# Kernel optimization log

Hardware: AMD Instinct MI355X
Metric: run time of the kernel (lower is better)

Reference implementation:

```python
import jax, jax.numpy as jnp
import numpy as np

QDIM = 1024; KDIM = 2048; NH = 16; HD = QDIM // NH
H = 64; W = 64; B = 8; S2 = 256
EPS = 1e-6; SCALE = HD ** -0.5


def setup_inputs() -> dict:
    key = jax.random.key(0)
    ks = jax.random.split(key, 8)
    def lin(k, fan_in, shape):
        lim = 1.0 / np.sqrt(fan_in)
        return jax.random.uniform(k, shape, jnp.float32, -lim, lim)
    return {
        "x": jax.random.normal(ks[0], (B, H * W, QDIM), jnp.float32),
        "y": jax.random.normal(ks[1], (B, S2, KDIM), jnp.float32),
        "wq": lin(ks[2], QDIM, (QDIM, QDIM)),
        "bq": lin(ks[3], QDIM, (QDIM,)),
        "wkv": lin(ks[4], KDIM, (2 * QDIM, KDIM)),
        "bkv": lin(ks[5], KDIM, (2 * QDIM,)),
        "wo": lin(ks[6], QDIM, (QDIM, QDIM)),
        "bo": lin(ks[7], QDIM, (QDIM,)),
        "qn_g": jnp.ones((HD,), jnp.float32),
        "qn_b": jnp.zeros((HD,), jnp.float32),
        "kn_g": jnp.ones((HD,), jnp.float32),
        "kn_b": jnp.zeros((HD,), jnp.float32),
    }


def _layernorm(t, g, b):
    mu = t.mean(-1, keepdims=True)
    var = ((t - mu) ** 2).mean(-1, keepdims=True)
    return (t - mu) * jax.lax.rsqrt(var + EPS) * g + b


def _rope_2d_angles():
    # Lumina-style 2D rotary: head_dim//2 complex freqs per position,
    # interleaving H-axis and W-axis frequencies along the pair dim.
    d4 = HD // 4
    inv = 1.0 / (10000.0 ** (np.arange(0, HD // 2, 2, dtype=np.float32) / (HD // 2)))  # (d4,)
    fh = np.outer(np.arange(H, dtype=np.float32), inv)  # (H, d4)
    fw = np.outer(np.arange(W, dtype=np.float32), inv)  # (W, d4)
    ang = np.stack([
        np.broadcast_to(fh[:, None, :], (H, W, d4)),
        np.broadcast_to(fw[None, :, :], (H, W, d4)),
    ], axis=-1).reshape(H, W, HD // 2)  # interleaved h,w,h,w,...
    return jnp.asarray(np.cos(ang)), jnp.asarray(np.sin(ang))


def reference(x, y, wq, bq, wkv, bkv, wo, bo, qn_g, qn_b, kn_g, kn_b):
    b, s1, c = x.shape
    q = (x @ wq.T + bq).reshape(b, s1, NH, HD).transpose(0, 2, 1, 3)          # (b, nh, s1, hd)
    kv = (y @ wkv.T + bkv).reshape(b, -1, 2, NH, HD).transpose(0, 2, 3, 1, 4)  # (b, 2, nh, s2, hd)
    k, v = kv[:, 0], kv[:, 1]
    q = _layernorm(q, qn_g, qn_b)
    k = _layernorm(k, kn_g, kn_b)
    # inline 2D RoPE on Q only (complex mult on interleaved pairs)
    cos, sin = _rope_2d_angles()                                               # (H, W, hd//2)
    qr = q.reshape(b, NH, H, W, HD // 2, 2)
    qe, qo = qr[..., 0], qr[..., 1]
    q = jnp.stack([qe * cos - qo * sin, qe * sin + qo * cos], axis=-1).reshape(b, NH, s1, HD)
    attn = jax.nn.softmax((q * SCALE) @ jnp.swapaxes(k, -2, -1), axis=-1)      # (b, nh, s1, s2)
    out = (attn @ v).transpose(0, 2, 1, 3).reshape(b, s1, c)
    return out @ wo.T + bo
```

## Files before the change

### kernel.cpp

```cpp
#include <hip/hip_runtime.h>
#include <hip/hip_bf16.h>

typedef __bf16 bf16x8 __attribute__((ext_vector_type(8)));
typedef __bf16 bf16x4 __attribute__((ext_vector_type(4)));
typedef float f32x4 __attribute__((ext_vector_type(4)));

__device__ __forceinline__ void async_copy16(__bf16* lds_base, const __bf16* g) {
  __builtin_amdgcn_global_load_lds(
      (const __attribute__((address_space(1))) void*)g,
      (__attribute__((address_space(3))) void*)lds_base, 16, 0, 0);
}

__global__ __launch_bounds__(256) void cvt_bf16(const float* __restrict__ in,
                                                __bf16* __restrict__ out, int n4) {
  int i = blockIdx.x * 256 + threadIdx.x;
  if (i >= n4) return;
  float4 v = ((const float4*)in)[i];
  bf16x4 o;
  o.x = (__bf16)v.x; o.y = (__bf16)v.y; o.z = (__bf16)v.z; o.w = (__bf16)v.w;
  ((bf16x4*)out)[i] = o;
}

template<bool STORE_BF16>
__global__ __launch_bounds__(256) void gemm_bt(const __bf16* __restrict__ A,
                                               const __bf16* __restrict__ Bw,
                                               const float* __restrict__ bias,
                                               void* __restrict__ Cp,
                                               int M, int N, int K) {
  __shared__ __align__(16) __bf16 sA[128 * 64];
  __shared__ __align__(16) __bf16 sB[128 * 64];
  const int tid = threadIdx.x;
  const int lane = tid & 63;
  const int w = tid >> 6;
  const int wr = w >> 1, wc = w & 1;
  const int l15 = lane & 15, q4 = lane >> 4;
  const int bm = blockIdx.x, bn = blockIdx.y;

  f32x4 acc[4][4] = {};

  for (int k0 = 0; k0 < K; k0 += 64) {
    __syncthreads();
#pragma unroll
    for (int it = 0; it < 4; ++it) {
      int chunk = it * 256 + tid;
      int row = chunk >> 3, c8 = chunk & 7;
      int ldsbase = (it * 256 + w * 64) * 8;
      async_copy16(sA + ldsbase, A + (size_t)(bm * 128 + row) * K + k0 + c8 * 8);
      async_copy16(sB + ldsbase, Bw + (size_t)(bn * 128 + row) * K + k0 + c8 * 8);
    }
    __syncthreads();
#pragma unroll
    for (int kk = 0; kk < 2; ++kk) {
      bf16x8 af[4], bfr[4];
#pragma unroll
      for (int i = 0; i < 4; ++i)
        af[i] = *(const bf16x8*)(sA + (wr * 64 + i * 16 + l15) * 64 + kk * 32 + q4 * 8);
#pragma unroll
      for (int j = 0; j < 4; ++j)
        bfr[j] = *(const bf16x8*)(sB + (wc * 64 + j * 16 + l15) * 64 + kk * 32 + q4 * 8);
#pragma unroll
      for (int i = 0; i < 4; ++i)
#pragma unroll
        for (int j = 0; j < 4; ++j)
          acc[i][j] = __builtin_amdgcn_mfma_f32_16x16x32_bf16(af[i], bfr[j], acc[i][j], 0, 0, 0);
    }
  }
#pragma unroll
  for (int j = 0; j < 4; ++j) {
    const int col = bn * 128 + wc * 64 + j * 16 + l15;
    const float bv = bias[col];
#pragma unroll
    for (int i = 0; i < 4; ++i) {
      const int row0 = bm * 128 + wr * 64 + i * 16 + q4 * 4;
#pragma unroll
      for (int r = 0; r < 4; ++r) {
        float v = acc[i][j][r] + bv;
        size_t off = (size_t)(row0 + r) * N + col;
        if (STORE_BF16) ((__bf16*)Cp)[off] = (__bf16)v;
        else            ((float*)Cp)[off]  = v;
      }
    }
  }
}

template<int KK, int EPI>
__global__ __launch_bounds__(512, 2) void gemm_big(const __bf16* __restrict__ A,
                                                   const __bf16* __restrict__ Bw,
                                                   const float* __restrict__ bias,
                                                   void* __restrict__ Cp,
                                                   const float* __restrict__ g,
                                                   const float* __restrict__ bt,
                                                   int N) {
  constexpr int NT = KK / 64;
  static_assert(NT >= 3, "need >=3 K-tiles");
  __shared__ __align__(16) __bf16 sA[2][256 * 64];
  __shared__ __align__(16) __bf16 sB[2][256 * 64];
  const int tid = threadIdx.x;
  const int lane = tid & 63;
  const int w = tid >> 6;
  const int wr = w >> 2, wc = w & 3;
  const int l15 = lane & 15, q4 = lane >> 4;
  const int bm = blockIdx.x, bn = blockIdx.y;

  const int rl = lane >> 3;
  const int cs = (lane & 7) ^ rl;
  const __bf16* Ag = A + (size_t)(bm * 256) * KK + cs * 8;
  const __bf16* Bg = Bw + (size_t)(bn * 256) * KK + cs * 8;
  const int gbA = w * 8;
  const int gbB = (w & 3) * 8 + (w >> 2) * 64;

  auto STAGE_A = [&](int bb, int t, int h) {
    int gb = gbA + h * 64;
    async_copy16(&sA[bb][gb * 64],         Ag + (size_t)(gb + rl) * KK + t * 64);
    async_copy16(&sA[bb][(gb + 128) * 64], Ag + (size_t)(gb + 128 + rl) * KK + t * 64);
  };
  auto STAGE_B = [&](int bb, int t, int h) {
    int gb = gbB + h * 32;
    async_copy16(&sB[bb][gb * 64],         Bg + (size_t)(gb + rl) * KK + t * 64);
    async_copy16(&sB[bb][(gb + 128) * 64], Bg + (size_t)(gb + 128 + rl) * KK + t * 64);
  };

  const int pc0 = ((q4) ^ (l15 & 7)) * 8;
  const int pc1 = ((4 + q4) ^ (l15 & 7)) * 8;
  const int arow0 = (wr * 128 + l15) * 64;
  const int brow0 = (wc * 64 + l15) * 64;

  f32x4 acc[8][4] = {};

  STAGE_A(0, 0, 0); STAGE_B(0, 0, 0); STAGE_B(0, 0, 1); STAGE_A(0, 0, 1);
  STAGE_A(1, 1, 0); STAGE_B(1, 1, 0);
  asm volatile("s_waitcnt vmcnt(4)" ::: "memory");
  __builtin_amdgcn_s_barrier();
  __builtin_amdgcn_sched_barrier(0);

#pragma unroll 2
  for (int t = 0; t < NT; ++t) {
    const int cb = t & 1, nb = cb ^ 1;
    const __bf16* sAc = sA[cb];
    const __bf16* sBc = sB[cb];
    bf16x8 a[4][2], b0[2][2], b1[2][2];

#pragma unroll
    for (int m = 0; m < 4; ++m) {
      a[m][0] = *(const bf16x8*)(sAc + arow0 + m * 1024 + pc0);
      a[m][1] = *(const bf16x8*)(sAc + arow0 + m * 1024 + pc1);
    }
#pragma unroll
    for (int n = 0; n < 2; ++n) {
      b0[n][0] = *(const bf16x8*)(sBc + brow0 + n * 1024 + pc0);
      b0[n][1] = *(const bf16x8*)(sBc + brow0 + n * 1024 + pc1);
    }
    if (t + 1 < NT) STAGE_B(nb, t + 1, 1);
    __builtin_amdgcn_s_barrier();
    asm volatile("s_waitcnt lgkmcnt(0)" ::: "memory");
    __builtin_amdgcn_sched_barrier(0);
    __builtin_amdgcn_s_setprio(1);
#pragma unroll
    for (int m = 0; m < 4; ++m)
#pragma unroll
      for (int n = 0; n < 2; ++n) {
        acc[m][n] = __builtin_amdgcn_mfma_f32_16x16x32_bf16(a[m][0], b0[n][0], acc[m][n], 0, 0, 0);
        acc[m][n] = __builtin_amdgcn_mfma_f32_16x16x32_bf16(a[m][1], b0[n][1], acc[m][n], 0, 0, 0);
      }
    __builtin_amdgcn_s_setprio(0);
    __builtin_amdgcn_s_barrier();
    __builtin_amdgcn_sched_barrier(0);

#pragma unroll
    for (int n = 0; n < 2; ++n) {
      b1[n][0] = *(const bf16x8*)(sBc + brow0 + (2 + n) * 1024 + pc0);
      b1[n][1] = *(const bf16x8*)(sBc + brow0 + (2 + n) * 1024 + pc1);
    }
    if (t + 1 < NT) STAGE_A(nb, t + 1, 1);
    __builtin_amdgcn_s_barrier();
    asm volatile("s_waitcnt lgkmcnt(0)" ::: "memory");
    __builtin_amdgcn_sched_barrier(0);
    __builtin_amdgcn_s_setprio(1);
#pragma unroll
    for (int m = 0; m < 4; ++m)
#pragma unroll
      for (int n = 0; n < 2; ++n) {
        acc[m][2 + n] = __builtin_amdgcn_mfma_f32_16x16x32_bf16(a[m][0], b1[n][0], acc[m][2 + n], 0, 0, 0);
        acc[m][2 + n] = __builtin_amdgcn_mfma_f32_16x16x32_bf16(a[m][1], b1[n][1], acc[m][2 + n], 0, 0, 0);
      }
    __builtin_amdgcn_s_setprio(0);
    __builtin_amdgcn_s_barrier();
    __builtin_amdgcn_sched_barrier(0);

#pragma unroll
    for (int m = 0; m < 4; ++m) {
      a[m][0] = *(const bf16x8*)(sAc + arow0 + (4 + m) * 1024 + pc0);
      a[m][1] = *(const bf16x8*)(sAc + arow0 + (4 + m) * 1024 + pc1);
    }
    if (t + 2 < NT) STAGE_A(cb, t + 2, 0);
    __builtin_amdgcn_s_barrier();
    asm volatile("s_waitcnt lgkmcnt(0)" ::: "memory");
    __builtin_amdgcn_sched_barrier(0);
    __builtin_amdgcn_s_setprio(1);
#pragma unroll
    for (int m = 0; m < 4; ++m)
#pragma unroll
      for (int n = 0; n < 2; ++n) {
        acc[4 + m][n] = __builtin_amdgcn_mfma_f32_16x16x32_bf16(a[m][0], b0[n][0], acc[4 + m][n], 0, 0, 0);
        acc[4 + m][n] = __builtin_amdgcn_mfma_f32_16x16x32_bf16(a[m][1], b0[n][1], acc[4 + m][n], 0, 0, 0);
      }
    __builtin_amdgcn_s_setprio(0);
    __builtin_amdgcn_s_barrier();
    __builtin_amdgcn_sched_barrier(0);

    if (t + 2 < NT) STAGE_B(cb, t + 2, 0);
    if (t + 2 < NT)      { asm volatile("s_waitcnt vmcnt(4)" ::: "memory"); }
    else if (t + 1 < NT) { asm volatile("s_waitcnt vmcnt(0)" ::: "memory"); }
    __builtin_amdgcn_s_barrier();
    __builtin_amdgcn_sched_barrier(0);
    __builtin_amdgcn_s_setprio(1);
#pragma unroll
    for (int m = 0; m < 4; ++m)
#pragma unroll
      for (int n = 0; n < 2; ++n) {
        acc[4 + m][2 + n] = __builtin_amdgcn_mfma_f32_16x16x32_bf16(a[m][0], b1[n][0], acc[4 + m][2 + n], 0, 0, 0);
        acc[4 + m][2 + n] = __builtin_amdgcn_mfma_f32_16x16x32_bf16(a[m][1], b1[n][1], acc[4 + m][2 + n], 0, 0, 0);
      }
    __builtin_amdgcn_s_setprio(0);
    __builtin_amdgcn_s_barrier();
    __builtin_amdgcn_sched_barrier(0);
  }

  if (EPI == 0) {
#pragma unroll
    for (int n = 0; n < 4; ++n) {
      const int col = bn * 256 + wc * 64 + n * 16 + l15;
      const float bv = bias[col];
#pragma unroll
      for (int m = 0; m < 8; ++m) {
        const int row0 = bm * 256 + wr * 128 + m * 16 + q4 * 4;
#pragma unroll
        for (int r = 0; r < 4; ++r)
          ((float*)Cp)[(size_t)(row0 + r) * N + col] = acc[m][n][r] + bv;
      }
    }
  } else {
    const int nh = bn * 4 + wc;
    const int usew = (l15 >> 1) & 1;
    const float sgn = (l15 & 1) ? 1.f : -1.f;
    float gq[4], bqv[4], inv[4], bv[4];
#pragma unroll
    for (int n = 0; n < 4; ++n) {
      const int d = n * 16 + l15;
      gq[n] = g[d]; bqv[n] = bt[d];
      bv[n] = bias[nh * 64 + d];
      inv[n] = __expf(-(float)(d >> 2) * 0.5756462732485114f);
    }
#pragma unroll
    for (int m = 0; m < 8; ++m) {
#pragma unroll
      for (int r = 0; r < 4; ++r) {
        const int row = bm * 256 + wr * 128 + m * 16 + q4 * 4 + r;
        const int s1 = row & 4095, bidx = row >> 12;
        const float base = usew ? (float)(s1 & 63) : (float)(s1 >> 6);
        float v[4];
        float sum = 0.f;
#pragma unroll
        for (int n = 0; n < 4; ++n) { v[n] = acc[m][n][r] + bv[n]; sum += v[n]; }
        sum += __shfl_xor(sum, 1); sum += __shfl_xor(sum, 2);
        sum += __shfl_xor(sum, 4); sum += __shfl_xor(sum, 8);
        const float mu = sum * (1.f / 64.f);
        float sq = 0.f;
#pragma unroll
        for (int n = 0; n < 4; ++n) { v[n] -= mu; sq += v[n] * v[n]; }
        sq += __shfl_xor(sq, 1); sq += __shfl_xor(sq, 2);
        sq += __shfl_xor(sq, 4); sq += __shfl_xor(sq, 8);
        const float rs = rsqrtf(sq * (1.f / 64.f) + 1e-6f);
        __bf16* Qrow = (__bf16*)Cp + ((size_t)(bidx * 16 + nh) * 4096 + s1) * 64;
#pragma unroll
        for (int n = 0; n < 4; ++n) {
          const float xn = v[n] * rs * gq[n] + bqv[n];
          const float ang = base * inv[n];
          const float cc = __cosf(ang), ssn = __sinf(ang);
          const float partner = __shfl_xor(xn, 1);
          const float rot = (xn * cc + partner * ssn * sgn) * 0.125f;
          Qrow[n * 16 + l15] = (__bf16)rot;
        }
      }
    }
  }
}

__global__ __launch_bounds__(256) void kv_epilogue(const float* __restrict__ kv,
                                                   const float* __restrict__ g,
                                                   const float* __restrict__ bta,
                                                   __bf16* __restrict__ Kd,
                                                   __bf16* __restrict__ VT) {
  const int lane = threadIdx.x & 63;
  const int vec = blockIdx.x * 4 + (threadIdx.x >> 6);
  const int nh = vec & 15;
  const int sv = (vec >> 4) & 1;
  const int row = vec >> 5;
  const int b = row >> 8, s2 = row & 255;
  float v = kv[(size_t)row * 2048 + sv * 1024 + nh * 64 + lane];
  if (sv == 0) {
    float mu = v;
#pragma unroll
    for (int o = 32; o; o >>= 1) mu += __shfl_xor(mu, o);
    mu *= (1.f / 64.f);
    float d = v - mu;
    float va = d * d;
#pragma unroll
    for (int o = 32; o; o >>= 1) va += __shfl_xor(va, o);
    va *= (1.f / 64.f);
    float xn = d * rsqrtf(va + 1e-6f) * g[lane] + bta[lane];
    Kd[(((size_t)b * 16 + nh) * 256 + s2) * 64 + lane] = (__bf16)xn;
  } else {
    VT[(((size_t)b * 16 + nh) * 64 + lane) * 256 + s2] = (__bf16)v;
  }
}

__global__ __launch_bounds__(256) void attn_kernel(const __bf16* __restrict__ Q,
                                                   const __bf16* __restrict__ Kd,
                                                   const __bf16* __restrict__ VT,
                                                   __bf16* __restrict__ O) {
  __shared__ __align__(16) __bf16 sK[256 * 64];
  __shared__ __align__(16) __bf16 sV[64 * 256];
  const int tid = threadIdx.x, lane = tid & 63, w = tid >> 6;
  const int l15 = lane & 15, q4 = lane >> 4;
  const int s7 = l15 & 7;
  const int bh = blockIdx.y;
  const int m0 = blockIdx.x * 64;
  const __bf16* Kg = Kd + (size_t)bh * 256 * 64;
  const __bf16* Vg = VT + (size_t)bh * 64 * 256;
  const __bf16* Qg = Q + ((size_t)bh * 4096 + m0) * 64;
#pragma unroll
  for (int it = 0; it < 8; ++it) {
    int c = it * 256 + tid;
    int kr = c >> 3, kh = c & 7;
    *(uint4*)(sK + kr * 64 + ((kh ^ (kr & 7)) * 8)) = *(const uint4*)(Kg + c * 8);
    int vr = c >> 5, vh = c & 31;
    *(uint4*)(sV + vr * 256 + ((vh ^ (vr & 7)) * 8)) = *(const uint4*)(Vg + c * 8);
  }
  bf16x8 qf0 = *(const bf16x8*)(Qg + (w * 16 + l15) * 64 + q4 * 8);
  bf16x8 qf1 = *(const bf16x8*)(Qg + (w * 16 + l15) * 64 + 32 + q4 * 8);
  __syncthreads();
  f32x4 sacc[16] = {};
#pragma unroll
  for (int mt = 0; mt < 16; ++mt) {
    bf16x8 a0 = *(const bf16x8*)(sK + (mt * 16 + l15) * 64 + ((q4 ^ s7) * 8));
    bf16x8 a1 = *(const bf16x8*)(sK + (mt * 16 + l15) * 64 + (((4 + q4) ^ s7) * 8));
    sacc[mt] = __builtin_amdgcn_mfma_f32_16x16x32_bf16(a0, qf0, sacc[mt], 0, 0, 0);
    sacc[mt] = __builtin_amdgcn_mfma_f32_16x16x32_bf16(a1, qf1, sacc[mt], 0, 0, 0);
  }
  __syncthreads();
  float mx = -1e30f;
#pragma unroll
  for (int mt = 0; mt < 16; ++mt)
#pragma unroll
    for (int r = 0; r < 4; ++r) mx = fmaxf(mx, sacc[mt][r]);
  mx = fmaxf(mx, __shfl_xor(mx, 16));
  mx = fmaxf(mx, __shfl_xor(mx, 32));
  float l = 0.f;
#pragma unroll
  for (int mt = 0; mt < 16; ++mt)
#pragma unroll
    for (int r = 0; r < 4; ++r) {
      float p = __expf(sacc[mt][r] - mx);
      sacc[mt][r] = p;
      l += p;
    }
  l += __shfl_xor(l, 16);
  l += __shfl_xor(l, 32);
  const float linv = 1.f / l;
#pragma unroll
  for (int mt = 0; mt < 16; ++mt) {
    bf16x4 pk;
    pk.x = (__bf16)(sacc[mt][0] * linv);
    pk.y = (__bf16)(sacc[mt][1] * linv);
    pk.z = (__bf16)(sacc[mt][2] * linv);
    pk.w = (__bf16)(sacc[mt][3] * linv);
    int chunk = mt * 2 + (q4 >> 1);
    *(bf16x4*)(sK + (w * 16 + l15) * 256 + ((chunk ^ s7) * 8) + (q4 & 1) * 4) = pk;
  }
  f32x4 oacc[4] = {};
#pragma unroll
  for (int ks = 0; ks < 8; ++ks) {
    int phys = ((ks * 4 + q4) ^ s7) * 8;
    bf16x8 a = *(const bf16x8*)(sK + (w * 16 + l15) * 256 + phys);
#pragma unroll
    for (int j = 0; j < 4; ++j) {
      bf16x8 b = *(const bf16x8*)(sV + (j * 16 + l15) * 256 + phys);
      oacc[j] = __builtin_amdgcn_mfma_f32_16x16x32_bf16(a, b, oacc[j], 0, 0, 0);
    }
  }
  const int b = bh >> 4, nh = bh & 15;
#pragma unroll
  for (int j = 0; j < 4; ++j)
#pragma unroll
    for (int r = 0; r < 4; ++r) {
      size_t off = ((size_t)b * 4096 + m0 + w * 16 + q4 * 4 + r) * 1024
                 + nh * 64 + j * 16 + l15;
      O[off] = (__bf16)oacc[j][r];
    }
}

extern "C" void kernel_launch(void* const* d_in, const int* in_sizes, int n_in,
                              void* d_out, int out_size, void* d_ws, size_t ws_size,
                              hipStream_t stream) {
  const float* x    = (const float*)d_in[0];
  const float* y    = (const float*)d_in[1];
  const float* wq   = (const float*)d_in[2];
  const float* bq   = (const float*)d_in[3];
  const float* wkv  = (const float*)d_in[4];
  const float* bkv  = (const float*)d_in[5];
  const float* wo   = (const float*)d_in[6];
  const float* bo   = (const float*)d_in[7];
  const float* qng  = (const float*)d_in[8];
  const float* qnb  = (const float*)d_in[9];
  const float* kng  = (const float*)d_in[10];
  const float* knb  = (const float*)d_in[11];
  float* out = (float*)d_out;

  char* ws = (char*)d_ws;
  size_t off = 0;
  auto take = [&](size_t bytes) { char* p = ws + off; off += (bytes + 255) & ~(size_t)255; return p; };
  __bf16* xb   = (__bf16*)take((size_t)32768 * 1024 * 2);
  char*  reg1  = take((size_t)32768 * 1024 * 2);
  __bf16* Qb   = (__bf16*)take((size_t)32768 * 1024 * 2);
  __bf16* yb   = (__bf16*)take((size_t)2048 * 2048 * 2);
  __bf16* wqb  = (__bf16*)take((size_t)1024 * 1024 * 2);
  __bf16* wkvb = (__bf16*)take((size_t)2048 * 2048 * 2);
  __bf16* wob  = (__bf16*)take((size_t)1024 * 1024 * 2);
  __bf16* Kb   = (__bf16*)take((size_t)128 * 256 * 64 * 2);
  __bf16* VTb  = (__bf16*)take((size_t)128 * 64 * 256 * 2);
  float*  kvf  = (float*)reg1;
  __bf16* aout = xb;

  cvt_bf16<<<32768, 256, 0, stream>>>(x,   xb,   8388608);
  cvt_bf16<<<4096,  256, 0, stream>>>(y,   yb,   1048576);
  cvt_bf16<<<1024,  256, 0, stream>>>(wq,  wqb,  262144);
  cvt_bf16<<<4096,  256, 0, stream>>>(wkv, wkvb, 1048576);
  cvt_bf16<<<1024,  256, 0, stream>>>(wo,  wob,  262144);

  gemm_bt<false><<<dim3(16, 16), 256, 0, stream>>>(yb, wkvb, bkv, kvf, 2048, 2048, 2048);
  kv_epilogue<<<16384, 256, 0, stream>>>(kvf, kng, knb, Kb, VTb);

  gemm_big<1024, 2><<<dim3(128, 4), 512, 0, stream>>>(xb, wqb, bq, Qb, qng, qnb, 1024);

  attn_kernel<<<dim3(64, 128), 256, 0, stream>>>(Qb, Kb, VTb, aout);

  gemm_big<1024, 0><<<dim3(128, 4), 512, 0, stream>>>(aout, wob, bo, out, nullptr, nullptr, 1024);
}
```

Measured before the change: 600.0 us.

## Prefetch B fragments, swizzle block order, stage Q epilogue through LDS

Merges the two shared buffers into one array so the Q epilogue can reuse it. Accumulators are written to LDS with an XOR swizzle, and each thread then handles a full 64-wide head row: LayerNorm with no cross-lane shuffles, RoPE, and 16-byte vectorized bf16 stores. The first B fragments of each K-tile are now loaded from LDS at the end of the previous iteration, hiding LDS latency before the MFMAs. The block index is also remapped so consecutive blocks interleave across the grid, aiming for better L2 reuse. The mapping hardcodes grid dimensions (128 columns, 4 bn) and so applies to every gemm_big instantiation, not only the Q projection; it is correct only for those grid sizes.

```diff
diff --git a/kernel.cpp b/kernel.cpp
--- a/kernel.cpp
+++ b/kernel.cpp
@@ -93,14 +93,16 @@
                                                    int N) {
   constexpr int NT = KK / 64;
   static_assert(NT >= 3, "need >=3 K-tiles");
-  __shared__ __align__(16) __bf16 sA[2][256 * 64];
-  __shared__ __align__(16) __bf16 sB[2][256 * 64];
+  __shared__ __align__(16) __bf16 smem[4 * 256 * 64];
   const int tid = threadIdx.x;
   const int lane = tid & 63;
   const int w = tid >> 6;
   const int wr = w >> 2, wc = w & 3;
   const int l15 = lane & 15, q4 = lane >> 4;
-  const int bm = blockIdx.x, bn = blockIdx.y;
+
+  const int bid = (blockIdx.y << 7) + blockIdx.x;
+  const int sbid = (bid & 7) * 64 + (bid >> 3);
+  const int bm = sbid >> 2, bn = sbid & 3;
 
   const int rl = lane >> 3;
   const int cs = (lane & 7) ^ rl;
@@ -109,15 +111,18 @@
   const int gbA = w * 8;
   const int gbB = (w & 3) * 8 + (w >> 2) * 64;
 
+  auto sAbuf = [&](int bb) { return smem + bb * 16384; };
+  auto sBbuf = [&](int bb) { return smem + 32768 + bb * 16384; };
+
   auto STAGE_A = [&](int bb, int t, int h) {
     int gb = gbA + h * 64;
-    async_copy16(&sA[bb][gb * 64],         Ag + (size_t)(gb + rl) * KK + t * 64);
-    async_copy16(&sA[bb][(gb + 128) * 64], Ag + (size_t)(gb + 128 + rl) * KK + t * 64);
+    async_copy16(sAbuf(bb) + gb * 64,         Ag + (size_t)(gb + rl) * KK + t * 64);
+    async_copy16(sAbuf(bb) + (gb + 128) * 64, Ag + (size_t)(gb + 128 + rl) * KK + t * 64);
   };
   auto STAGE_B = [&](int bb, int t, int h) {
     int gb = gbB + h * 32;
-    async_copy16(&sB[bb][gb * 64],         Bg + (size_t)(gb + rl) * KK + t * 64);
-    async_copy16(&sB[bb][(gb + 128) * 64], Bg + (size_t)(gb + 128 + rl) * KK + t * 64);
+    async_copy16(sBbuf(bb) + gb * 64,         Bg + (size_t)(gb + rl) * KK + t * 64);
+    async_copy16(sBbuf(bb) + (gb + 128) * 64, Bg + (size_t)(gb + 128 + rl) * KK + t * 64);
   };
 
   const int pc0 = ((q4) ^ (l15 & 7)) * 8;
@@ -126,30 +131,31 @@
   const int brow0 = (wc * 64 + l15) * 64;
 
   f32x4 acc[8][4] = {};
+  bf16x8 b0[2][2];
 
   STAGE_A(0, 0, 0); STAGE_B(0, 0, 0); STAGE_B(0, 0, 1); STAGE_A(0, 0, 1);
   STAGE_A(1, 1, 0); STAGE_B(1, 1, 0);
   asm volatile("s_waitcnt vmcnt(4)" ::: "memory");
   __builtin_amdgcn_s_barrier();
   __builtin_amdgcn_sched_barrier(0);
+#pragma unroll
+  for (int n = 0; n < 2; ++n) {
+    b0[n][0] = *(const bf16x8*)(sBbuf(0) + brow0 + n * 1024 + pc0);
+    b0[n][1] = *(const bf16x8*)(sBbuf(0) + brow0 + n * 1024 + pc1);
+  }
 
 #pragma unroll 2
   for (int t = 0; t < NT; ++t) {
     const int cb = t & 1, nb = cb ^ 1;
-    const __bf16* sAc = sA[cb];
-    const __bf16* sBc = sB[cb];
-    bf16x8 a[4][2], b0[2][2], b1[2][2];
+    const __bf16* sAc = sAbuf(cb);
+    const __bf16* sBc = sBbuf(cb);
+    bf16x8 a[4][2], b1[2][2];
 
 #pragma unroll
     for (int m = 0; m < 4; ++m) {
       a[m][0] = *(const bf16x8*)(sAc + arow0 + m * 1024 + pc0);
       a[m][1] = *(const bf16x8*)(sAc + arow0 + m * 1024 + pc1);
     }
-#pragma unroll
-    for (int n = 0; n < 2; ++n) {
-      b0[n][0] = *(const bf16x8*)(sBc + brow0 + n * 1024 + pc0);
-      b0[n][1] = *(const bf16x8*)(sBc + brow0 + n * 1024 + pc1);
-    }
     if (t + 1 < NT) STAGE_B(nb, t + 1, 1);
     __builtin_amdgcn_s_barrier();
     asm volatile("s_waitcnt lgkmcnt(0)" ::: "memory");
@@ -213,6 +219,14 @@
     else if (t + 1 < NT) { asm volatile("s_waitcnt vmcnt(0)" ::: "memory"); }
     __builtin_amdgcn_s_barrier();
     __builtin_amdgcn_sched_barrier(0);
+    if (t + 1 < NT) {
+      const __bf16* sBn = sBbuf(nb);
+#pragma unroll
+      for (int n = 0; n < 2; ++n) {
+        b0[n][0] = *(const bf16x8*)(sBn + brow0 + n * 1024 + pc0);
+        b0[n][1] = *(const bf16x8*)(sBn + brow0 + n * 1024 + pc1);
+      }
+    }
     __builtin_amdgcn_s_setprio(1);
 #pragma unroll
     for (int m = 0; m < 4; ++m)
@@ -240,47 +254,73 @@
       }
     }
   } else {
-    const int nh = bn * 4 + wc;
-    const int usew = (l15 >> 1) & 1;
-    const float sgn = (l15 & 1) ? 1.f : -1.f;
-    float gq[4], bqv[4], inv[4], bv[4];
-#pragma unroll
-    for (int n = 0; n < 4; ++n) {
-      const int d = n * 16 + l15;
-      gq[n] = g[d]; bqv[n] = bt[d];
-      bv[n] = bias[nh * 64 + d];
-      inv[n] = __expf(-(float)(d >> 2) * 0.5756462732485114f);
-    }
-#pragma unroll
-    for (int m = 0; m < 8; ++m) {
-#pragma unroll
-      for (int r = 0; r < 4; ++r) {
-        const int row = bm * 256 + wr * 128 + m * 16 + q4 * 4 + r;
-        const int s1 = row & 4095, bidx = row >> 12;
-        const float base = usew ? (float)(s1 & 63) : (float)(s1 >> 6);
-        float v[4];
-        float sum = 0.f;
-#pragma unroll
-        for (int n = 0; n < 4; ++n) { v[n] = acc[m][n][r] + bv[n]; sum += v[n]; }
-        sum += __shfl_xor(sum, 1); sum += __shfl_xor(sum, 2);
-        sum += __shfl_xor(sum, 4); sum += __shfl_xor(sum, 8);
-        const float mu = sum * (1.f / 64.f);
-        float sq = 0.f;
-#pragma unroll
-        for (int n = 0; n < 4; ++n) { v[n] -= mu; sq += v[n] * v[n]; }
-        sq += __shfl_xor(sq, 1); sq += __shfl_xor(sq, 2);
-        sq += __shfl_xor(sq, 4); sq += __shfl_xor(sq, 8);
-        const float rs = rsqrtf(sq * (1.f / 64.f) + 1e-6f);
-        __bf16* Qrow = (__bf16*)Cp + ((size_t)(bidx * 16 + nh) * 4096 + s1) * 64;
-#pragma unroll
-        for (int n = 0; n < 4; ++n) {
-          const float xn = v[n] * rs * gq[n] + bqv[n];
-          const float ang = base * inv[n];
-          const float cc = __cosf(ang), ssn = __sinf(ang);
-          const float partner = __shfl_xor(xn, 1);
-          const float rot = (xn * cc + partner * ssn * sgn) * 0.125f;
-          Qrow[n * 16 + l15] = (__bf16)rot;
+    float* sf = (float*)smem;
+    float bv[4];
+#pragma unroll
+    for (int n = 0; n < 4; ++n) bv[n] = bias[bn * 256 + wc * 64 + n * 16 + l15];
+    const int hh = tid & 3, rr = tid >> 2;
+    const int nh = bn * 4 + hh;
+    const int rkey = rr & 7;
+#pragma unroll
+    for (int p = 0; p < 2; ++p) {
+      __builtin_amdgcn_s_barrier();
+      if (wr == p) {
+#pragma unroll
+        for (int m = 0; m < 8; ++m)
+#pragma unroll
+          for (int r = 0; r < 4; ++r) {
+            const int row = m * 16 + q4 * 4 + r;
+            const int key = row & 7;
+#pragma unroll
+            for (int n = 0; n < 4; ++n) {
+              const int chunk = wc * 16 + n * 4 + (l15 >> 2);
+              sf[row * 256 + ((chunk ^ key) << 2) + (l15 & 3)] = acc[m][n][r] + bv[n];
+            }
+          }
+      }
+      __builtin_amdgcn_s_barrier();
+      const int grow = bm * 256 + p * 128 + rr;
+      const int s1 = grow & 4095, bidx = grow >> 12;
+      const float hp = (float)(s1 >> 6), wp = (float)(s1 & 63);
+      const float* rbase = sf + rr * 256;
+      f32x4 vv[16];
+      float sum = 0.f;
+#pragma unroll
+      for (int j = 0; j < 16; ++j) {
+        vv[j] = *(const f32x4*)(rbase + (((hh * 16 + j) ^ rkey) << 2));
+#pragma unroll
+        for (int e = 0; e < 4; ++e) sum += vv[j][e];
+      }
+      const float mu = sum * (1.f / 64.f);
+      float sq = 0.f;
+#pragma unroll
+      for (int j = 0; j < 16; ++j)
+#pragma unroll
+        for (int e = 0; e < 4; ++e) { float d = vv[j][e] - mu; sq += d * d; }
+      const float rs = rsqrtf(sq * (1.f / 64.f) + 1e-6f);
+      __bf16* Qrow = (__bf16*)Cp + (((size_t)bidx * 16 + nh) * 4096 + s1) * 64;
+#pragma unroll
+      for (int j2 = 0; j2 < 8; ++j2) {
+        bf16x8 o;
+#pragma unroll
+        for (int h2 = 0; h2 < 2; ++h2) {
+          const int j = j2 * 2 + h2;
+          const f32x4 gv  = *(const f32x4*)(g + j * 4);
+          const f32x4 btv = *(const f32x4*)(bt + j * 4);
+          const float x0 = (vv[j][0] - mu) * rs * gv[0] + btv[0];
+          const float x1 = (vv[j][1] - mu) * rs * gv[1] + btv[1];
+          const float x2 = (vv[j][2] - mu) * rs * gv[2] + btv[2];
+          const float x3 = (vv[j][3] - mu) * rs * gv[3] + btv[3];
+          const float inv = __expf(-(float)j * 0.5756462732485114f);
+          const float a0 = hp * inv, a1 = wp * inv;
+          const float c0 = __cosf(a0), s0 = __sinf(a0);
+          const float c1 = __cosf(a1), s1v = __sinf(a1);
+          o[h2 * 4 + 0] = (__bf16)((x0 * c0 - x1 * s0) * 0.125f);
+          o[h2 * 4 + 1] = (__bf16)((x0 * s0 + x1 * c0) * 0.125f);
+          o[h2 * 4 + 2] = (__bf16)((x2 * c1 - x3 * s1v) * 0.125f);
+          o[h2 * 4 + 3] = (__bf16)((x2 * s1v + x3 * c1) * 0.125f);
         }
+        *(bf16x8*)(Qrow + j2 * 8) = o;
       }
     }
   }
```

New measurement: 611.8 us. About the same (+2.0%).
